# Kernel optimization log

Measured on AMD Instinct MI355X. Metric: run time of the kernel, lower is better.

The kernel has to match this reference:

```python
import jax, jax.numpy as jnp
import numpy as np

N, E, H, D_IN, D_EDGE, L = 20000, 320000, 128, 128, 32, 4
EPS = 1e-5

def setup_inputs() -> dict:
    key = jax.random.key(0)
    ks = jax.random.split(key, 16)
    d_in_edge = 2 * H + 1 + D_EDGE  # cat[h_row, h_col, radial, edge_attr] (input_nf==hidden here)
    s = 0.02
    inp = {
        'h': jax.random.normal(ks[0], (N, D_IN), jnp.float32),
        'coords': jax.random.normal(ks[1], (N, 3), jnp.float32),
        'edge_attr': jax.random.normal(ks[2], (E, D_EDGE), jnp.float32),
        'edges': jax.random.randint(ks[3], (2, E), 0, N),
        'edge_w1': jax.random.normal(ks[4], (L, d_in_edge, H), jnp.float32) * s,
        'edge_b1': jnp.zeros((L, H), jnp.float32),
        'edge_w2': jax.random.normal(ks[5], (L, H, H), jnp.float32) * s,
        'edge_b2': jnp.zeros((L, H), jnp.float32),
        'node_w1': jax.random.normal(ks[6], (L, H + H, H), jnp.float32) * s,
        'node_b1': jnp.zeros((L, H), jnp.float32),
        'node_w2': jax.random.normal(ks[7], (L, H, H), jnp.float32) * s,
        'node_b2': jnp.zeros((L, H), jnp.float32),
        'ln_g': jnp.ones((H,), jnp.float32),
        'ln_b': jnp.zeros((H,), jnp.float32),
    }
    return inp

def _egnn(h, coords, edge_attr, edges, ew1, eb1, ew2, eb2, nw1, nb1, nw2, nb2, ln_g, ln_b):
    row, col = edges[0], edges[1]
    # squared-distance radial feature; coords are not updated across layers
    # (EGNN.forward discards coordinate updates: h, _, _ = layer(...)).
    diff = coords[row] - coords[col]              # [E,3]
    radial = jnp.sum(diff * diff, axis=-1, keepdims=True)  # [E,1]
    for i in range(L):
        hr, hc = h[row], h[col]                   # gathers [E,H]
        m = jnp.concatenate([hr, hc, radial, edge_attr], axis=-1)
        m = jax.nn.silu(m @ ew1[i] + eb1[i])      # [E,H]
        m = jax.nn.silu(m @ ew2[i] + eb2[i])      # [E,H]
        agg = jax.ops.segment_sum(m, row, num_segments=N)  # scatter-add [N,H]
        z = jnp.concatenate([h, agg], axis=-1)    # [N,2H]
        out = jax.nn.silu(z @ nw1[i] + nb1[i]) @ nw2[i] + nb2[i]
        h = out if i == 0 else h + out            # layer 0 non-recurrent
    mu = jnp.mean(h, axis=-1, keepdims=True)
    var = jnp.mean((h - mu) ** 2, axis=-1, keepdims=True)
    return (h - mu) * jax.lax.rsqrt(var + EPS) * ln_g + ln_b

def reference(h, coords, edge_attr, edges, edge_w1, edge_b1, edge_w2, edge_b2,
              node_w1, node_b1, node_w2, node_b2, ln_g, ln_b):
    return _egnn(h, coords, edge_attr, edges, edge_w1, edge_b1, edge_w2, edge_b2,
                 node_w1, node_b1, node_w2, node_b2, ln_g, ln_b)
```

## Files before the change

### kernel.cpp

```cpp
#include <hip/hip_runtime.h>
#include <hip/hip_bf16.h>

#define NN 20000
#define EE 320000
#define HH 128
#define DE 32
#define LL 4

typedef __bf16 bf16_t;
typedef __bf16 bf16x8 __attribute__((ext_vector_type(8)));
typedef float f32x4 __attribute__((ext_vector_type(4)));

static __device__ __forceinline__ float silu_f(float x) {
    return x * __builtin_amdgcn_rcpf(1.f + __expf(-x));
}

static __device__ __forceinline__ int permrow(int el) {
    return ((el >> 2) & 3) * 16 + ((el >> 4) & 3) * 4 + (el & 3);
}

__global__ void prep_weights(const float* __restrict__ ew1, const float* __restrict__ eb1f,
                             const float* __restrict__ ew2,
                             const float* __restrict__ nw1, const float* __restrict__ nw2,
                             bf16_t* __restrict__ WPT, bf16_t* __restrict__ W1C,
                             bf16_t* __restrict__ W2T, bf16_t* __restrict__ N1T,
                             bf16_t* __restrict__ N2T)
{
    int i = blockIdx.x * 256 + threadIdx.x;
    const int SW = LL * 256 * 128;
    if (i < SW) {
        int l = i / (256 * 128), r = i % (256 * 128);
        int c = r / 128, k = r % 128;
        int krow = (c < 128) ? k : 128 + k;
        WPT[i] = (bf16_t)ew1[((size_t)l * 289 + krow) * 128 + (c & 127)];
        return;
    }
    i -= SW;
    const int SC = LL * 128 * 64;
    if (i < SC) {
        int l = i / (128 * 64), r = i % (128 * 64);
        int c = r / 64, kk = r % 64;
        float v;
        if (kk == 0)       v = ew1[((size_t)l * 289 + 256) * 128 + c];
        else if (kk <= 32) v = ew1[((size_t)l * 289 + 256 + kk) * 128 + c];
        else if (kk == 33) v = eb1f[l * 128 + c];
        else               v = 0.f;
        W1C[i] = (bf16_t)v;
        return;
    }
    i -= SC;
    const int S2 = LL * 128 * 128;
    if (i < S2) {
        int l = i / (128 * 128), r = i % (128 * 128);
        int n = r / 128, k = r % 128;
        W2T[i] = (bf16_t)ew2[((size_t)l * 128 + k) * 128 + n];
        return;
    }
    i -= S2;
    const int S3 = LL * 128 * 256;
    if (i < S3) {
        int l = i / (128 * 256), r = i % (128 * 256);
        int n = r / 256, k = r % 256;
        N1T[i] = (bf16_t)nw1[((size_t)l * 256 + k) * 128 + n];
        return;
    }
    i -= S3;
    if (i < S2) {
        int l = i / (128 * 128), r = i % (128 * 128);
        int n = r / 128, k = r % 128;
        N2T[i] = (bf16_t)nw2[((size_t)l * 128 + k) * 128 + n];
    }
}

__global__ void hist_kernel(const int* __restrict__ edges, int* __restrict__ counts)
{
    int e = blockIdx.x * 256 + threadIdx.x;
    if (e < EE) atomicAdd(&counts[edges[e]], 1);
}

__global__ void scan_kernel(const int* __restrict__ counts, int* __restrict__ starts)
{
    __shared__ int wsum[16];
    __shared__ int running_s;
    const int tid = threadIdx.x;
    const int lane = tid & 63, wv = tid >> 6;
    if (tid == 0) running_s = 0;
    __syncthreads();
    for (int base = 0; base < NN; base += 1024) {
        int i = base + tid;
        int v = (i < NN) ? counts[i] : 0;
        int orig = v;
        #pragma unroll
        for (int off = 1; off < 64; off <<= 1) {
            int t = __shfl_up(v, off);
            if (lane >= off) v += t;
        }
        if (lane == 63) wsum[wv] = v;
        __syncthreads();
        if (tid < 16) {
            int s = wsum[tid];
            #pragma unroll
            for (int off = 1; off < 16; off <<= 1) {
                int t = __shfl_up(s, off);
                if (tid >= off) s += t;
            }
            wsum[tid] = s;
        }
        __syncthreads();
        int waveoff = (wv == 0) ? 0 : wsum[wv - 1];
        if (i < NN) starts[i] = running_s + waveoff + v - orig;
        int total = wsum[15];
        __syncthreads();
        if (tid == 0) running_s += total;
        __syncthreads();
    }
}

__global__ void scatter_kernel(const int* __restrict__ edges, int* __restrict__ cursor,
                               int* __restrict__ eidx, int* __restrict__ row_s,
                               int* __restrict__ col_s)
{
    int e = blockIdx.x * 256 + threadIdx.x;
    if (e >= EE) return;
    int r = edges[e], c = edges[EE + e];
    int pos = atomicAdd(&cursor[r], 1);
    eidx[pos] = e;
    row_s[pos] = r;
    col_s[pos] = c;
}

__global__ void build_re(const int* __restrict__ eidx, const int* __restrict__ row_s,
                         const int* __restrict__ col_s, const float* __restrict__ coords,
                         const float* __restrict__ ea, bf16_t* __restrict__ RE)
{
    int pos = blockIdx.x * 256 + threadIdx.x;
    if (pos >= EE) return;
    int e = eidx[pos], r = row_s[pos], c = col_s[pos];
    float dx = coords[r * 3 + 0] - coords[c * 3 + 0];
    float dy = coords[r * 3 + 1] - coords[c * 3 + 1];
    float dz = coords[r * 3 + 2] - coords[c * 3 + 2];
    alignas(16) bf16_t buf[40];
    buf[0] = (bf16_t)(dx * dx + dy * dy + dz * dz);
    #pragma unroll
    for (int j = 0; j < 32; ++j) buf[1 + j] = (bf16_t)ea[(size_t)e * DE + j];
    buf[33] = (bf16_t)1.0f;
    #pragma unroll
    for (int j = 34; j < 40; ++j) buf[j] = (bf16_t)0.f;
    bf16x8* dst = (bf16x8*)(RE + (size_t)pos * 40);
    #pragma unroll
    for (int k = 0; k < 5; ++k) dst[k] = ((const bf16x8*)buf)[k];
}

__global__ __launch_bounds__(256, 2) void node_pre(
    const float* __restrict__ h, const bf16_t* __restrict__ WPT,
    bf16_t* __restrict__ P, int layer)
{
    __shared__ bf16_t Hs[64][136];
    const int tid = threadIdx.x;
    const int n0 = blockIdx.x * 64;
    {
        const int nl = tid >> 2, q = tid & 3;
        const int node = n0 + nl;
        if (node < NN) {
            const float* hp = h + (size_t)node * HH;
            #pragma unroll
            for (int j = 0; j < 8; ++j) {
                float4 v = *(const float4*)(hp + q * 32 + j * 4);
                int k = q * 32 + j * 4;
                Hs[nl][k + 0] = (bf16_t)v.x; Hs[nl][k + 1] = (bf16_t)v.y;
                Hs[nl][k + 2] = (bf16_t)v.z; Hs[nl][k + 3] = (bf16_t)v.w;
            }
        } else {
            #pragma unroll
            for (int j = 0; j < 8; ++j) {
                int k = q * 32 + j * 4;
                Hs[nl][k] = (bf16_t)0.f; Hs[nl][k + 1] = (bf16_t)0.f;
                Hs[nl][k + 2] = (bf16_t)0.f; Hs[nl][k + 3] = (bf16_t)0.f;
            }
        }
    }
    __syncthreads();

    const int lane = tid & 63, w = tid >> 6;
    const int ln = lane & 15, kg = lane >> 4;

    f32x4 acc[4][4] = {};
    const bf16_t* Wl = WPT + (size_t)layer * 256 * 128;
    #pragma unroll
    for (int kt = 0; kt < 4; ++kt) {
        const int kb = kt * 32 + kg * 8;
        bf16x8 a[4], b[4];
        #pragma unroll
        for (int m = 0; m < 4; ++m) a[m] = *(const bf16x8*)&Hs[m * 16 + ln][kb];
        #pragma unroll
        for (int n = 0; n < 4; ++n)
            b[n] = *(const bf16x8*)(Wl + (size_t)(w * 64 + n * 16 + ln) * 128 + kb);
        #pragma unroll
        for (int m = 0; m < 4; ++m)
            #pragma unroll
            for (int n = 0; n < 4; ++n)
                acc[m][n] = __builtin_amdgcn_mfma_f32_16x16x32_bf16(a[m], b[n], acc[m][n], 0, 0, 0);
    }
    #pragma unroll
    for (int n = 0; n < 4; ++n) {
        int col = w * 64 + n * 16 + ln;
        #pragma unroll
        for (int m = 0; m < 4; ++m)
            #pragma unroll
            for (int rr = 0; rr < 4; ++rr) {
                int node = n0 + m * 16 + kg * 4 + rr;
                if (node < NN) P[(size_t)node * 256 + col] = (bf16_t)acc[m][n][rr];
            }
    }
}

__global__ __launch_bounds__(256, 4) void edge_kernel(
    const bf16_t* __restrict__ P, const bf16_t* __restrict__ RE,
    const int* __restrict__ row_s, const int* __restrict__ col_s,
    const bf16_t* __restrict__ W1C, const bf16_t* __restrict__ W2T,
    const float* __restrict__ b2, float* __restrict__ agg, int layer)
{
    __shared__ bf16_t pABs[64][136];
    __shared__ bf16_t bufM[64][136];
    __shared__ int rows_l[64];

    const int tid = threadIdx.x;
    const int e0 = blockIdx.x * 64;

    if (tid < 64) rows_l[tid] = row_s[e0 + permrow(tid)];

    {
        const int el = tid >> 2, q = tid & 3;
        const int es = e0 + permrow(el);
        const bf16_t* src = RE + (size_t)es * 40;
        bf16x8 z = {};
        if (q < 2) {
            *(bf16x8*)&bufM[el][q * 16]     = *(const bf16x8*)(src + q * 16);
            *(bf16x8*)&bufM[el][q * 16 + 8] = *(const bf16x8*)(src + q * 16 + 8);
        } else if (q == 2) {
            *(bf16x8*)&bufM[el][32] = *(const bf16x8*)(src + 32);
            *(bf16x8*)&bufM[el][40] = z;
        } else {
            *(bf16x8*)&bufM[el][48] = z;
            *(bf16x8*)&bufM[el][56] = z;
        }
    }
    {
        const int el = tid >> 2, q = tid & 3;
        const int es = e0 + permrow(el);
        int r = row_s[es], c = col_s[es];
        const bf16_t* pa = P + (size_t)r * 256 + q * 32;
        const bf16_t* pb = P + (size_t)c * 256 + 128 + q * 32;
        #pragma unroll
        for (int j = 0; j < 4; ++j) {
            bf16x8 va = *(const bf16x8*)(pa + j * 8);
            bf16x8 vb = *(const bf16x8*)(pb + j * 8);
            bf16x8 o;
            #pragma unroll
            for (int t = 0; t < 8; ++t) o[t] = (bf16_t)((float)va[t] + (float)vb[t]);
            *(bf16x8*)&pABs[el][q * 32 + j * 8] = o;
        }
    }
    __syncthreads();

    const int lane = tid & 63, w = tid >> 6;
    const int ln = lane & 15, kg = lane >> 4;

    f32x4 acc[4][2] = {};
    const bf16_t* W1l = W1C + (size_t)layer * 128 * 64;
    #pragma unroll
    for (int kt = 0; kt < 2; ++kt) {
        const int kb = kt * 32 + kg * 8;
        bf16x8 a[4], b[2];
        #pragma unroll
        for (int m = 0; m < 4; ++m) a[m] = *(const bf16x8*)&bufM[m * 16 + ln][kb];
        #pragma unroll
        for (int n = 0; n < 2; ++n)
            b[n] = *(const bf16x8*)(W1l + (size_t)(w * 32 + n * 16 + ln) * 64 + kb);
        #pragma unroll
        for (int m = 0; m < 4; ++m)
            #pragma unroll
            for (int n = 0; n < 2; ++n)
                acc[m][n] = __builtin_amdgcn_mfma_f32_16x16x32_bf16(a[m], b[n], acc[m][n], 0, 0, 0);
    }
    __syncthreads();

    #pragma unroll
    for (int n = 0; n < 2; ++n) {
        int col = w * 32 + n * 16 + ln;
        #pragma unroll
        for (int m = 0; m < 4; ++m)
            #pragma unroll
            for (int rr = 0; rr < 4; ++rr) {
                int er = m * 16 + kg * 4 + rr;
                float x = acc[m][n][rr] + (float)pABs[er][col];
                bufM[er][col] = (bf16_t)silu_f(x);
            }
    }
    __syncthreads();

    f32x4 acc2[4][2] = {};
    const bf16_t* W2l = W2T + (size_t)layer * 128 * 128;
    #pragma unroll
    for (int kt = 0; kt < 4; ++kt) {
        const int kb = kt * 32 + kg * 8;
        bf16x8 a[4], b[2];
        #pragma unroll
        for (int m = 0; m < 4; ++m) a[m] = *(const bf16x8*)&bufM[m * 16 + ln][kb];
        #pragma unroll
        for (int n = 0; n < 2; ++n)
            b[n] = *(const bf16x8*)(W2l + (size_t)(w * 32 + n * 16 + ln) * 128 + kb);
        #pragma unroll
        for (int m = 0; m < 4; ++m)
            #pragma unroll
            for (int n = 0; n < 2; ++n)
                acc2[m][n] = __builtin_amdgcn_mfma_f32_16x16x32_bf16(a[m], b[n], acc2[m][n], 0, 0, 0);
    }

    {
        int myrow[16];
        #pragma unroll
        for (int m = 0; m < 4; ++m)
            #pragma unroll
            for (int rr = 0; rr < 4; ++rr)
                myrow[m * 4 + rr] = rows_l[m * 16 + kg * 4 + rr];

        #pragma unroll
        for (int n = 0; n < 2; ++n) {
            int col = w * 32 + n * 16 + ln;
            float bias = b2[layer * 128 + col];
            float s = 0.f;
            int cur = myrow[0];
            #pragma unroll
            for (int m = 0; m < 4; ++m) {
                #pragma unroll
                for (int rr = 0; rr < 4; ++rr) {
                    int r = myrow[m * 4 + rr];
                    float v = silu_f(acc2[m][n][rr] + bias);
                    if (r != cur) {
                        atomicAdd(&agg[(size_t)cur * HH + col], s);
                        s = 0.f; cur = r;
                    }
                    s += v;
                }
            }
            atomicAdd(&agg[(size_t)cur * HH + col], s);
        }
    }
}

__global__ __launch_bounds__(256, 2) void node_kernel(
    float* __restrict__ h, const float* __restrict__ agg,
    const bf16_t* __restrict__ N1T, const float* __restrict__ b1,
    const bf16_t* __restrict__ N2T, const float* __restrict__ b2,
    int layer)
{
    __shared__ bf16_t Zs[64][264];
    __shared__ bf16_t M1s[64][136];

    const int tid = threadIdx.x;
    const int n0 = blockIdx.x * 64;

    {
        const int nl = tid >> 2, q = tid & 3;
        const int node = n0 + nl;
        if (node < NN) {
            const float* hp = h + (size_t)node * HH;
            const float* ap = agg + (size_t)node * HH;
            #pragma unroll
            for (int kk = 0; kk < 64; kk += 4) {
                int k = q * 64 + kk;
                float4 v = (k < 128) ? *(const float4*)(hp + k)
                                     : *(const float4*)(ap + (k - 128));
                Zs[nl][k + 0] = (bf16_t)v.x; Zs[nl][k + 1] = (bf16_t)v.y;
                Zs[nl][k + 2] = (bf16_t)v.z; Zs[nl][k + 3] = (bf16_t)v.w;
            }
        } else {
            #pragma unroll
            for (int kk = 0; kk < 64; kk += 4) {
                int k = q * 64 + kk;
                Zs[nl][k + 0] = (bf16_t)0.f; Zs[nl][k + 1] = (bf16_t)0.f;
                Zs[nl][k + 2] = (bf16_t)0.f; Zs[nl][k + 3] = (bf16_t)0.f;
            }
        }
    }
    __syncthreads();

    const int lane = tid & 63, w = tid >> 6;
    const int ln = lane & 15, kg = lane >> 4;

    f32x4 acc[4][2] = {};
    const bf16_t* N1l = N1T + (size_t)layer * 128 * 256;
    #pragma unroll
    for (int kt = 0; kt < 8; ++kt) {
        const int kb = kt * 32 + kg * 8;
        bf16x8 a[4], b[2];
        #pragma unroll
        for (int m = 0; m < 4; ++m) a[m] = *(const bf16x8*)&Zs[m * 16 + ln][kb];
        #pragma unroll
        for (int n = 0; n < 2; ++n)
            b[n] = *(const bf16x8*)(N1l + (size_t)(w * 32 + n * 16 + ln) * 256 + kb);
        #pragma unroll
        for (int m = 0; m < 4; ++m)
            #pragma unroll
            for (int n = 0; n < 2; ++n)
                acc[m][n] = __builtin_amdgcn_mfma_f32_16x16x32_bf16(a[m], b[n], acc[m][n], 0, 0, 0);
    }

    #pragma unroll
    for (int n = 0; n < 2; ++n) {
        int col = w * 32 + n * 16 + ln;
        float bias = b1[layer * 128 + col];
        #pragma unroll
        for (int m = 0; m < 4; ++m)
            #pragma unroll
            for (int rr = 0; rr < 4; ++rr) {
                float x = acc[m][n][rr] + bias;
                M1s[m * 16 + kg * 4 + rr][col] = (bf16_t)silu_f(x);
            }
    }
    __syncthreads();

    f32x4 acc2[4][2] = {};
    const bf16_t* N2l = N2T + (size_t)layer * 128 * 128;
    #pragma unroll
    for (int kt = 0; kt < 4; ++kt) {
        const int kb = kt * 32 + kg * 8;
        bf16x8 a[4], b[2];
        #pragma unroll
        for (int m = 0; m < 4; ++m) a[m] = *(const bf16x8*)&M1s[m * 16 + ln][kb];
        #pragma unroll
        for (int n = 0; n < 2; ++n)
            b[n] = *(const bf16x8*)(N2l + (size_t)(w * 32 + n * 16 + ln) * 128 + kb);
        #pragma unroll
        for (int m = 0; m < 4; ++m)
            #pragma unroll
            for (int n = 0; n < 2; ++n)
                acc2[m][n] = __builtin_amdgcn_mfma_f32_16x16x32_bf16(a[m], b[n], acc2[m][n], 0, 0, 0);
    }

    #pragma unroll
    for (int n = 0; n < 2; ++n) {
        int col = w * 32 + n * 16 + ln;
        float bias = b2[layer * 128 + col];
        #pragma unroll
        for (int m = 0; m < 4; ++m)
            #pragma unroll
            for (int rr = 0; rr < 4; ++rr) {
                int node = n0 + m * 16 + kg * 4 + rr;
                if (node < NN) {
                    float x = acc2[m][n][rr] + bias;
                    float* hp = &h[(size_t)node * HH + col];
                    float res = (layer == 0) ? 0.f : *hp;
                    *hp = res + x;
                }
            }
    }
}

__global__ void ln_kernel(float* __restrict__ h, const float* __restrict__ g,
                          const float* __restrict__ bb)
{
    int node = blockIdx.x * 4 + (threadIdx.x >> 6);
    int lane = threadIdx.x & 63;
    if (node >= NN) return;
    float* hp = h + (size_t)node * HH;
    float v0 = hp[lane], v1 = hp[lane + 64];
    float s = v0 + v1, sq = v0 * v0 + v1 * v1;
    #pragma unroll
    for (int o = 32; o; o >>= 1) {
        s  += __shfl_xor(s, o);
        sq += __shfl_xor(sq, o);
    }
    float mu  = s * (1.f / 128.f);
    float var = sq * (1.f / 128.f) - mu * mu;
    float inv = rsqrtf(var + 1e-5f);
    hp[lane]      = (v0 - mu) * inv * g[lane]      + bb[lane];
    hp[lane + 64] = (v1 - mu) * inv * g[lane + 64] + bb[lane + 64];
}

extern "C" void kernel_launch(void* const* d_in, const int* in_sizes, int n_in,
                              void* d_out, int out_size, void* d_ws, size_t ws_size,
                              hipStream_t stream)
{
    (void)in_sizes; (void)n_in; (void)out_size; (void)ws_size;

    const float* h_in    = (const float*)d_in[0];
    const float* coords  = (const float*)d_in[1];
    const float* ea      = (const float*)d_in[2];
    const int*   edges   = (const int*)d_in[3];
    const float* ew1     = (const float*)d_in[4];
    const float* eb1     = (const float*)d_in[5];
    const float* ew2     = (const float*)d_in[6];
    const float* eb2     = (const float*)d_in[7];
    const float* nw1     = (const float*)d_in[8];
    const float* nb1     = (const float*)d_in[9];
    const float* nw2     = (const float*)d_in[10];
    const float* nb2     = (const float*)d_in[11];
    const float* ln_g    = (const float*)d_in[12];
    const float* ln_b    = (const float*)d_in[13];

    char* ws = (char*)d_ws;
    int*    counts = (int*)(ws + 0);
    int*    starts = (int*)(ws + 80128);
    int*    cursor = (int*)(ws + 160384);
    int*    eidx   = (int*)(ws + 240512);
    int*    row_s  = (int*)(ws + 1520512);
    int*    col_s  = (int*)(ws + 2800512);
    bf16_t* RE     = (bf16_t*)(ws + 4080512);
    bf16_t* P      = (bf16_t*)(ws + 29680512);
    float*  agg    = (float*)(ws + 39920512);
    bf16_t* WPT    = (bf16_t*)(ws + 50160512);
    bf16_t* W1C    = (bf16_t*)(ws + 50422656);
    bf16_t* W2T    = (bf16_t*)(ws + 50488192);
    bf16_t* N1T    = (bf16_t*)(ws + 50619264);
    bf16_t* N2T    = (bf16_t*)(ws + 50881408);

    float* h = (float*)d_out;

    hipMemcpyAsync(h, h_in, (size_t)NN * HH * sizeof(float),
                   hipMemcpyDeviceToDevice, stream);
    prep_weights<<<1664, 256, 0, stream>>>(ew1, eb1, ew2, nw1, nw2,
                                           WPT, W1C, W2T, N1T, N2T);

    hipMemsetAsync(counts, 0, NN * sizeof(int), stream);
    hist_kernel<<<(EE + 255) / 256, 256, 0, stream>>>(edges, counts);
    scan_kernel<<<1, 1024, 0, stream>>>(counts, starts);
    hipMemcpyAsync(cursor, starts, NN * sizeof(int),
                   hipMemcpyDeviceToDevice, stream);
    scatter_kernel<<<(EE + 255) / 256, 256, 0, stream>>>(edges, cursor, eidx, row_s, col_s);
    build_re<<<(EE + 255) / 256, 256, 0, stream>>>(eidx, row_s, col_s, coords, ea, RE);

    for (int l = 0; l < LL; ++l) {
        node_pre<<<(NN + 63) / 64, 256, 0, stream>>>(h, WPT, P, l);
        hipMemsetAsync(agg, 0, (size_t)NN * HH * sizeof(float), stream);
        edge_kernel<<<EE / 64, 256, 0, stream>>>(P, RE, row_s, col_s,
                                                 W1C, W2T, eb2, agg, l);
        node_kernel<<<(NN + 63) / 64, 256, 0, stream>>>(h, agg, N1T, nb1, N2T, nb2, l);
    }
    ln_kernel<<<NN / 4, 256, 0, stream>>>(h, ln_g, ln_b);
}
```

Measured before the change: 458.1 us.

## Fuse next-layer node projection into node kernel and shrink edge kernel LDS

The per-layer node_pre projection is folded into the tail of the node kernel: the freshly computed h tile is written into shared memory and multiplied by the next layer's projection weights, removing one launch and a reread of h per layer. The initial device-to-device copy of h is dropped by reading h_in directly on layer 0. The edge kernel reuses pABs for the hidden activations, uses a smaller RE buffer, removes one barrier, and raises launch bounds to 6 blocks per CU to improve occupancy. It also reads row indices straight from global memory instead of staging them in shared memory. The costs are more register pressure in the node kernel and possible spills in the edge kernel.

```diff
diff --git a/kernel.cpp b/kernel.cpp
--- a/kernel.cpp
+++ b/kernel.cpp
@@ -214,20 +214,17 @@
     }
 }
 
-__global__ __launch_bounds__(256, 4) void edge_kernel(
+__global__ __launch_bounds__(256, 6) void edge_kernel(
     const bf16_t* __restrict__ P, const bf16_t* __restrict__ RE,
     const int* __restrict__ row_s, const int* __restrict__ col_s,
     const bf16_t* __restrict__ W1C, const bf16_t* __restrict__ W2T,
     const float* __restrict__ b2, float* __restrict__ agg, int layer)
 {
     __shared__ bf16_t pABs[64][136];
-    __shared__ bf16_t bufM[64][136];
-    __shared__ int rows_l[64];
+    __shared__ bf16_t REb[64][72];
 
     const int tid = threadIdx.x;
     const int e0 = blockIdx.x * 64;
-
-    if (tid < 64) rows_l[tid] = row_s[e0 + permrow(tid)];
 
     {
         const int el = tid >> 2, q = tid & 3;
@@ -235,14 +232,14 @@
         const bf16_t* src = RE + (size_t)es * 40;
         bf16x8 z = {};
         if (q < 2) {
-            *(bf16x8*)&bufM[el][q * 16]     = *(const bf16x8*)(src + q * 16);
-            *(bf16x8*)&bufM[el][q * 16 + 8] = *(const bf16x8*)(src + q * 16 + 8);
+            *(bf16x8*)&REb[el][q * 16]     = *(const bf16x8*)(src + q * 16);
+            *(bf16x8*)&REb[el][q * 16 + 8] = *(const bf16x8*)(src + q * 16 + 8);
         } else if (q == 2) {
-            *(bf16x8*)&bufM[el][32] = *(const bf16x8*)(src + 32);
-            *(bf16x8*)&bufM[el][40] = z;
+            *(bf16x8*)&REb[el][32] = *(const bf16x8*)(src + 32);
+            *(bf16x8*)&REb[el][40] = z;
         } else {
-            *(bf16x8*)&bufM[el][48] = z;
-            *(bf16x8*)&bufM[el][56] = z;
+            *(bf16x8*)&REb[el][48] = z;
+            *(bf16x8*)&REb[el][56] = z;
         }
     }
     {
@@ -273,7 +270,7 @@
         const int kb = kt * 32 + kg * 8;
         bf16x8 a[4], b[2];
         #pragma unroll
-        for (int m = 0; m < 4; ++m) a[m] = *(const bf16x8*)&bufM[m * 16 + ln][kb];
+        for (int m = 0; m < 4; ++m) a[m] = *(const bf16x8*)&REb[m * 16 + ln][kb];
         #pragma unroll
         for (int n = 0; n < 2; ++n)
             b[n] = *(const bf16x8*)(W1l + (size_t)(w * 32 + n * 16 + ln) * 64 + kb);
@@ -283,7 +280,6 @@
             for (int n = 0; n < 2; ++n)
                 acc[m][n] = __builtin_amdgcn_mfma_f32_16x16x32_bf16(a[m], b[n], acc[m][n], 0, 0, 0);
     }
-    __syncthreads();
 
     #pragma unroll
     for (int n = 0; n < 2; ++n) {
@@ -294,7 +290,7 @@
             for (int rr = 0; rr < 4; ++rr) {
                 int er = m * 16 + kg * 4 + rr;
                 float x = acc[m][n][rr] + (float)pABs[er][col];
-                bufM[er][col] = (bf16_t)silu_f(x);
+                pABs[er][col] = (bf16_t)silu_f(x);
             }
     }
     __syncthreads();
@@ -306,7 +302,7 @@
         const int kb = kt * 32 + kg * 8;
         bf16x8 a[4], b[2];
         #pragma unroll
-        for (int m = 0; m < 4; ++m) a[m] = *(const bf16x8*)&bufM[m * 16 + ln][kb];
+        for (int m = 0; m < 4; ++m) a[m] = *(const bf16x8*)&pABs[m * 16 + ln][kb];
         #pragma unroll
         for (int n = 0; n < 2; ++n)
             b[n] = *(const bf16x8*)(W2l + (size_t)(w * 32 + n * 16 + ln) * 128 + kb);
@@ -319,11 +315,15 @@
 
     {
         int myrow[16];
-        #pragma unroll
-        for (int m = 0; m < 4; ++m)
-            #pragma unroll
-            for (int rr = 0; rr < 4; ++rr)
-                myrow[m * 4 + rr] = rows_l[m * 16 + kg * 4 + rr];
+        {
+            const int4* rp = (const int4*)(row_s + e0 + kg * 16);
+            #pragma unroll
+            for (int j = 0; j < 4; ++j) {
+                int4 v = rp[j];
+                myrow[j * 4 + 0] = v.x; myrow[j * 4 + 1] = v.y;
+                myrow[j * 4 + 2] = v.z; myrow[j * 4 + 3] = v.w;
+            }
+        }
 
         #pragma unroll
         for (int n = 0; n < 2; ++n) {
@@ -349,11 +349,13 @@
     }
 }
 
-__global__ __launch_bounds__(256, 2) void node_kernel(
-    float* __restrict__ h, const float* __restrict__ agg,
+__global__ __launch_bounds__(256, 2) void node_fused(
+    const float* __restrict__ hin, float* __restrict__ hout,
+    const float* __restrict__ agg,
     const bf16_t* __restrict__ N1T, const float* __restrict__ b1,
     const bf16_t* __restrict__ N2T, const float* __restrict__ b2,
-    int layer)
+    const bf16_t* __restrict__ WPT, bf16_t* __restrict__ P,
+    int layer, int produceP)
 {
     __shared__ bf16_t Zs[64][264];
     __shared__ bf16_t M1s[64][136];
@@ -365,7 +367,7 @@
         const int nl = tid >> 2, q = tid & 3;
         const int node = n0 + nl;
         if (node < NN) {
-            const float* hp = h + (size_t)node * HH;
+            const float* hp = hin + (size_t)node * HH;
             const float* ap = agg + (size_t)node * HH;
             #pragma unroll
             for (int kk = 0; kk < 64; kk += 4) {
@@ -448,13 +450,45 @@
             #pragma unroll
             for (int rr = 0; rr < 4; ++rr) {
                 int node = n0 + m * 16 + kg * 4 + rr;
+                float x = acc2[m][n][rr] + bias;
                 if (node < NN) {
-                    float x = acc2[m][n][rr] + bias;
-                    float* hp = &h[(size_t)node * HH + col];
-                    float res = (layer == 0) ? 0.f : *hp;
-                    *hp = res + x;
+                    if (layer != 0) x += hin[(size_t)node * HH + col];
+                    hout[(size_t)node * HH + col] = x;
                 }
-            }
+                Zs[m * 16 + kg * 4 + rr][col] = (bf16_t)x;
+            }
+    }
+
+    if (produceP) {
+        __syncthreads();
+        f32x4 accP[4][4] = {};
+        const bf16_t* Wl = WPT + (size_t)(layer + 1) * 256 * 128;
+        #pragma unroll
+        for (int kt = 0; kt < 4; ++kt) {
+            const int kb = kt * 32 + kg * 8;
+            bf16x8 a[4], b[4];
+            #pragma unroll
+            for (int m = 0; m < 4; ++m) a[m] = *(const bf16x8*)&Zs[m * 16 + ln][kb];
+            #pragma unroll
+            for (int n = 0; n < 4; ++n)
+                b[n] = *(const bf16x8*)(Wl + (size_t)(w * 64 + n * 16 + ln) * 128 + kb);
+            #pragma unroll
+            for (int m = 0; m < 4; ++m)
+                #pragma unroll
+                for (int n = 0; n < 4; ++n)
+                    accP[m][n] = __builtin_amdgcn_mfma_f32_16x16x32_bf16(a[m], b[n], accP[m][n], 0, 0, 0);
+        }
+        #pragma unroll
+        for (int n = 0; n < 4; ++n) {
+            int col = w * 64 + n * 16 + ln;
+            #pragma unroll
+            for (int m = 0; m < 4; ++m)
+                #pragma unroll
+                for (int rr = 0; rr < 4; ++rr) {
+                    int node = n0 + m * 16 + kg * 4 + rr;
+                    if (node < NN) P[(size_t)node * 256 + col] = (bf16_t)accP[m][n][rr];
+                }
+        }
     }
 }
 
@@ -518,8 +552,6 @@
 
     float* h = (float*)d_out;
 
-    hipMemcpyAsync(h, h_in, (size_t)NN * HH * sizeof(float),
-                   hipMemcpyDeviceToDevice, stream);
     prep_weights<<<1664, 256, 0, stream>>>(ew1, eb1, ew2, nw1, nw2,
                                            WPT, W1C, W2T, N1T, N2T);
 
@@ -531,12 +563,15 @@
     scatter_kernel<<<(EE + 255) / 256, 256, 0, stream>>>(edges, cursor, eidx, row_s, col_s);
     build_re<<<(EE + 255) / 256, 256, 0, stream>>>(eidx, row_s, col_s, coords, ea, RE);
 
+    node_pre<<<(NN + 63) / 64, 256, 0, stream>>>(h_in, WPT, P, 0);
+
     for (int l = 0; l < LL; ++l) {
-        node_pre<<<(NN + 63) / 64, 256, 0, stream>>>(h, WPT, P, l);
         hipMemsetAsync(agg, 0, (size_t)NN * HH * sizeof(float), stream);
         edge_kernel<<<EE / 64, 256, 0, stream>>>(P, RE, row_s, col_s,
                                                  W1C, W2T, eb2, agg, l);
-        node_kernel<<<(NN + 63) / 64, 256, 0, stream>>>(h, agg, N1T, nb1, N2T, nb2, l);
+        node_fused<<<(NN + 63) / 64, 256, 0, stream>>>(
+            (l == 0) ? h_in : h, h, agg, N1T, nb1, N2T, nb2,
+            WPT, P, l, (l < LL - 1) ? 1 : 0);
     }
     ln_kernel<<<NN / 4, 256, 0, stream>>>(h, ln_g, ln_b);
 }
```

After: 423.3 us. 7.6% less time.
